# Kernel optimization log

Measured on AMD Instinct MI355X. Metric: run time of the kernel, lower is better.

The kernel has to match this reference:

```python
import jax, jax.numpy as jnp
import numpy as np

B, T, D, H, O = 32, 2048, 256, 512, 256


def setup_inputs() -> dict:
    key = jax.random.key(0)
    ks = jax.random.split(key, 8)
    s = lambda k, shp, fan: jax.random.normal(k, shp, dtype=jnp.float32) / np.sqrt(fan)
    return {
        "x": jax.random.normal(ks[0], (B, T, D), dtype=jnp.float32),
        "h0": jax.random.normal(ks[1], (1, B, H), dtype=jnp.float32),
        "W_ih": s(ks[2], (H, D), D),
        "W_hh": s(ks[3], (H, H), H),
        "b_ih": jnp.zeros((H,), jnp.float32),
        "b_hh": jnp.zeros((H,), jnp.float32),
        "W_lin": s(ks[4], (O, H), H),
        "b_lin": jnp.zeros((O,), jnp.float32),
    }


def reference(x, h0, W_ih, W_hh, b_ih, b_hh, W_lin, b_lin):
    # rnn_act == 'linear' branch: h_t = x_t @ W_ih^T + h_{t-1} @ W_hh^T + b_ih + b_hh
    h_init = h0[0]  # [B, H]
    # Precompute the input contribution for all timesteps at once: [B, T, H]
    xw = jnp.einsum("btd,hd->bth", x, W_ih) + (b_ih + b_hh)

    def step(h, xw_t):  # xw_t: [B, H]
        h_new = xw_t + h @ W_hh.T
        return h_new, h_new

    # scan over time axis
    _, z_t = jax.lax.scan(step, h_init, jnp.swapaxes(xw, 0, 1))  # [T, B, H]
    z = jnp.swapaxes(z_t, 0, 1)  # [B, T, H]

    logits = jnp.einsum("bth,oh->bto", z, W_lin) + b_lin
    out = jax.nn.softmax(logits, axis=2)
    return out, z
```

## Files before the change

kernel.cpp:

```cpp
#include <hip/hip_runtime.h>
#include <math.h>

#define B_ 32
#define T_ 2048
#define D_ 256
#define H_ 512
#define O_ 256
#define S_CH 8
#define C_CH 256

typedef short bf16x8 __attribute__((ext_vector_type(8)));
typedef float f32x4  __attribute__((ext_vector_type(4)));

#define NTL(p)     __builtin_nontemporal_load(p)

__device__ __forceinline__ unsigned short f2bf_rne(float x) {
    unsigned int u = __builtin_bit_cast(unsigned int, x);
    unsigned int r = (u + 0x7fffu + ((u >> 16) & 1u)) >> 16;
    return (unsigned short)r;
}
__device__ __forceinline__ float bf2f(unsigned short h) {
    unsigned int u = ((unsigned int)h) << 16;
    return __builtin_bit_cast(float, u);
}

#define MFMA16(a, b, c) __builtin_amdgcn_mfma_f32_16x16x32_bf16((a), (b), (c), 0, 0, 0)

__device__ __forceinline__ void split_frag(const float* p, bf16x8& hi, bf16x8& lo) {
    f32x4 a = *(const f32x4*)p;
    f32x4 b = *(const f32x4*)(p + 4);
#pragma unroll
    for (int i = 0; i < 4; i++) {
        unsigned short h = f2bf_rne(a[i]);
        hi[i] = (short)h; lo[i] = (short)f2bf_rne(a[i] - bf2f(h));
        unsigned short h2 = f2bf_rne(b[i]);
        hi[4 + i] = (short)h2; lo[4 + i] = (short)f2bf_rne(b[i] - bf2f(h2));
    }
}
__device__ __forceinline__ void split_frag_nt(const float* p, bf16x8& hi, bf16x8& lo) {
    f32x4 a = NTL((const f32x4*)p);
    f32x4 b = NTL((const f32x4*)(p + 4));
#pragma unroll
    for (int i = 0; i < 4; i++) {
        unsigned short h = f2bf_rne(a[i]);
        hi[i] = (short)h; lo[i] = (short)f2bf_rne(a[i] - bf2f(h));
        unsigned short h2 = f2bf_rne(b[i]);
        hi[4 + i] = (short)h2; lo[4 + i] = (short)f2bf_rne(b[i] - bf2f(h2));
    }
}

__device__ __forceinline__ size_t wpack_off(int n, int k, int KB) {
    int n16 = n >> 4, l15 = n & 15;
    int kb = k >> 5, lhi = (k >> 3) & 3, j = k & 7;
    return (((size_t)(n16 * KB + kb) * 4 + lhi) * 16 + l15) * 8 + j;
}

__device__ __forceinline__ int hfrag_off(int m, int n) {
    int m16 = m >> 4, l15m = m & 15;
    int kb = n >> 5, lhi = (n >> 3) & 3, j = n & 7;
    return (((m16 * 16 + kb) * 4 + lhi) * 16 + l15m) * 8 + j;
}

__global__ void k_pack(const float* __restrict__ in, unsigned short* __restrict__ hi,
                       unsigned short* __restrict__ lo, unsigned short* __restrict__ hi2,
                       unsigned short* __restrict__ lo2, int total, int kshift) {
    int i = blockIdx.x * 256 + threadIdx.x;
    if (i < total) {
        int n = i >> kshift;
        int k = i & ((1 << kshift) - 1);
        float v = in[i];
        unsigned short h = f2bf_rne(v);
        unsigned short l = f2bf_rne(v - bf2f(h));
        size_t o = wpack_off(n, k, 1 << (kshift - 5));
        hi[o] = h;
        lo[o] = l;
        if (hi2) { hi2[o] = h; lo2[o] = l; }
    }
}

__device__ __forceinline__ void mul_body(const float* __restrict__ A,
                                         const float* __restrict__ Bm,
                                         float* __restrict__ Out,
                                         unsigned short* __restrict__ d1h,
                                         unsigned short* __restrict__ d1l,
                                         unsigned short* __restrict__ d2h,
                                         unsigned short* __restrict__ d2l,
                                         float (*As)[33], float (*Bs)[33]) {
    int tx = threadIdx.x & 15, ty = threadIdx.x >> 4;
    int j0 = blockIdx.x * 32, i0 = blockIdx.y * 32;
    float a00 = 0.f, a01 = 0.f, a10 = 0.f, a11 = 0.f;
    int r  = threadIdx.x >> 3;
    int c4 = (threadIdx.x & 7) * 4;
    for (int kb = 0; kb < H_ / 32; kb++) {
        f32x4 va = *(const f32x4*)(A + (size_t)(i0 + r) * H_ + kb * 32 + c4);
        f32x4 vb = *(const f32x4*)(Bm + (size_t)(kb * 32 + r) * H_ + j0 + c4);
        __syncthreads();
        As[r][c4 + 0] = va[0]; As[r][c4 + 1] = va[1]; As[r][c4 + 2] = va[2]; As[r][c4 + 3] = va[3];
        Bs[r][c4 + 0] = vb[0]; Bs[r][c4 + 1] = vb[1]; Bs[r][c4 + 2] = vb[2]; Bs[r][c4 + 3] = vb[3];
        __syncthreads();
#pragma unroll
        for (int k = 0; k < 32; k++) {
            float b0 = Bs[k][tx * 2], b1 = Bs[k][tx * 2 + 1];
            float a0 = As[ty * 2][k], a1 = As[ty * 2 + 1][k];
            a00 += a0 * b0; a01 += a0 * b1; a10 += a1 * b0; a11 += a1 * b1;
        }
    }
    float vals[4] = {a00, a01, a10, a11};
#pragma unroll
    for (int q = 0; q < 4; q++) {
        int n = i0 + ty * 2 + (q >> 1);
        int k = j0 + tx * 2 + (q & 1);
        Out[(size_t)n * H_ + k] = vals[q];
        unsigned short h = f2bf_rne(vals[q]);
        unsigned short l = f2bf_rne(vals[q] - bf2f(h));
        size_t o = wpack_off(n, k, 16);
        if (d1h) { d1h[o] = h; d1l[o] = l; }
        if (d2h) { d2h[o] = h; d2l[o] = l; }
    }
}

__global__ __launch_bounds__(256) void k_mul(const float* __restrict__ A,
                                             const float* __restrict__ Bm,
                                             float* __restrict__ Out,
                                             unsigned short* __restrict__ d1h,
                                             unsigned short* __restrict__ d1l,
                                             unsigned short* __restrict__ d2h,
                                             unsigned short* __restrict__ d2l) {
    __shared__ float As[32][33];
    __shared__ float Bs[32][33];
    mul_body(A, Bm, Out, d1h, d1l, d2h, d2l, As, Bs);
}

__global__ __launch_bounds__(256) void k_mul_l2(const float* __restrict__ Whh,
                                                float* __restrict__ ws,
                                                unsigned short* __restrict__ Pp_hi,
                                                unsigned short* __restrict__ Pp_lo) {
    __shared__ float As[32][33];
    __shared__ float Bs[32][33];
    size_t HH = (size_t)H_ * H_;
    if (blockIdx.z == 0)
        mul_body(Whh, ws, ws + HH, Pp_hi + 2 * HH, Pp_lo + 2 * HH, nullptr, nullptr, As, Bs);
    else
        mul_body(ws, ws, ws + 2 * HH, Pp_hi + 3 * HH, Pp_lo + 3 * HH, nullptr, nullptr, As, Bs);
}

__global__ __launch_bounds__(256) void k_mul_l3(const float* __restrict__ Whh,
                                                float* __restrict__ ws,
                                                unsigned short* __restrict__ Pp_hi,
                                                unsigned short* __restrict__ Pp_lo,
                                                unsigned short* __restrict__ Qp_hi,
                                                unsigned short* __restrict__ Qp_lo) {
    __shared__ float As[32][33];
    __shared__ float Bs[32][33];
    size_t HH = (size_t)H_ * H_;
    float* M0 = ws;
    float* M1 = ws + HH;
    float* M2 = ws + 2 * HH;
    int z = blockIdx.z;
    if (z == 0)
        mul_body(Whh, M2, ws + 3 * HH, Pp_hi + 4 * HH, Pp_lo + 4 * HH, nullptr, nullptr, As, Bs);
    else if (z == 1)
        mul_body(M0, M2, ws + 4 * HH, Pp_hi + 5 * HH, Pp_lo + 5 * HH, nullptr, nullptr, As, Bs);
    else if (z == 2)
        mul_body(M1, M2, ws + 5 * HH, Pp_hi + 6 * HH, Pp_lo + 6 * HH, nullptr, nullptr, As, Bs);
    else
        mul_body(M2, M2, ws + 6 * HH, Pp_hi + 7 * HH, Pp_lo + 7 * HH, Qp_hi, Qp_lo, As, Bs);
}

__global__ void k_seed(const float* __restrict__ h0, const float* __restrict__ zb,
                       float* __restrict__ Va) {
    int i = blockIdx.x * 256 + threadIdx.x;
    int c = i >> 14;
    int bn = i & 16383;
    int b = bn >> 9, n = bn & 511;
    Va[i] = (c == 0) ? h0[bn] : zb[((size_t)b * T_ + (c * S_CH - 1)) * H_ + n];
}

__global__ __launch_bounds__(1024) void k_scan2(const float* __restrict__ Vin,
                                                const unsigned short* __restrict__ Qp_hi,
                                                const unsigned short* __restrict__ Qp_lo,
                                                float* __restrict__ Vout, int s) {
    __shared__ __attribute__((aligned(16))) unsigned short hA[16384];
    __shared__ __attribute__((aligned(16))) unsigned short lA[16384];
    int c = blockIdx.x;
    int w = threadIdx.x >> 6;
    int lane = threadIdx.x & 63;
    int l15 = lane & 15, lhi = lane >> 4;

    if (c < s) {
        size_t base = (size_t)c * B_ * H_;
        for (int i = threadIdx.x * 4; i < B_ * H_; i += 4096) {
            f32x4 v = *(const f32x4*)(Vin + base + i);
            *(f32x4*)(Vout + base + i) = v;
        }
        return;
    }

    size_t src = (size_t)(c - s) * B_ * H_;
    for (int i = threadIdx.x; i < 16384; i += 1024) {
        float v = Vin[src + i];
        int m = i >> 9, n = i & 511;
        unsigned short hi = f2bf_rne(v);
        int o = hfrag_off(m, n);
        hA[o] = hi;
        lA[o] = f2bf_rne(v - bf2f(hi));
    }
    __syncthreads();

    size_t dst = (size_t)c * B_ * H_;
    float ad[2][2][4];
#pragma unroll
    for (int mt = 0; mt < 2; mt++)
#pragma unroll
        for (int nt = 0; nt < 2; nt++) {
            int n = w * 32 + nt * 16 + l15;
#pragma unroll
            for (int r = 0; r < 4; r++) {
                int m = mt * 16 + lhi * 4 + r;
                ad[mt][nt][r] = Vin[dst + (size_t)m * H_ + n];
            }
        }

    f32x4 acc[2][2];
#pragma unroll
    for (int mt = 0; mt < 2; mt++)
#pragma unroll
        for (int nt = 0; nt < 2; nt++) acc[mt][nt] = (f32x4){0.f, 0.f, 0.f, 0.f};

    for (int kb = 0; kb < 16; kb++) {
        bf16x8 ah0 = *(const bf16x8*)&hA[(kb << 9) + lane * 8];
        bf16x8 ah1 = *(const bf16x8*)&hA[((16 + kb) << 9) + lane * 8];
        bf16x8 al0 = *(const bf16x8*)&lA[(kb << 9) + lane * 8];
        bf16x8 al1 = *(const bf16x8*)&lA[((16 + kb) << 9) + lane * 8];
#pragma unroll
        for (int nt = 0; nt < 2; nt++) {
            size_t wb = (((size_t)(w * 2 + nt) * 16 + kb) << 9) + lane * 8;
            bf16x8 bh = *(const bf16x8*)(Qp_hi + wb);
            bf16x8 bl = *(const bf16x8*)(Qp_lo + wb);
            acc[0][nt] = MFMA16(ah0, bh, acc[0][nt]);
            acc[0][nt] = MFMA16(al0, bh, acc[0][nt]);
            acc[0][nt] = MFMA16(ah0, bl, acc[0][nt]);
            acc[1][nt] = MFMA16(ah1, bh, acc[1][nt]);
            acc[1][nt] = MFMA16(al1, bh, acc[1][nt]);
            acc[1][nt] = MFMA16(ah1, bl, acc[1][nt]);
        }
    }
#pragma unroll
    for (int mt = 0; mt < 2; mt++)
#pragma unroll
        for (int nt = 0; nt < 2; nt++) {
            int n = w * 32 + nt * 16 + l15;
#pragma unroll
            for (int r = 0; r < 4; r++) {
                int m = mt * 16 + lhi * 4 + r;
                Vout[dst + (size_t)m * H_ + n] = acc[mt][nt][r] + ad[mt][nt][r];
            }
        }
}

__global__ __launch_bounds__(512) void k_xw(const float* __restrict__ x,
                                            const unsigned short* __restrict__ Wp_hi,
                                            const unsigned short* __restrict__ Wp_lo,
                                            const float* __restrict__ bih,
                                            const float* __restrict__ bhh,
                                            float* __restrict__ zb) {
    int b  = blockIdx.y;
    int t0 = blockIdx.x * 64;
    int w    = threadIdx.x >> 6;
    int lane = threadIdx.x & 63;
    int l15 = lane & 15, lhi = lane >> 4;
    int nb = w * 64;

    f32x4 acc[4][4];
    for (int mt = 0; mt < 4; mt++)
        for (int nt = 0; nt < 4; nt++)
            acc[mt][nt] = (f32x4){0.f, 0.f, 0.f, 0.f};

    const float* xb = x + (size_t)b * T_ * D_;
    for (int kb = 0; kb < D_ / 32; kb++) {
        int kofs = kb * 32 + lhi * 8;
        bf16x8 ah[4], al[4];
#pragma unroll
        for (int mt = 0; mt < 4; mt++) {
            int t = t0 + mt * 16 + l15;
            split_frag_nt(xb + (size_t)t * D_ + kofs, ah[mt], al[mt]);
        }
#pragma unroll
        for (int nt = 0; nt < 4; nt++) {
            size_t wb = (((size_t)(w * 4 + nt) * 8 + kb) << 9) + lane * 8;
            bf16x8 bh = *(const bf16x8*)(Wp_hi + wb);
            bf16x8 bl = *(const bf16x8*)(Wp_lo + wb);
#pragma unroll
            for (int mt = 0; mt < 4; mt++) {
                acc[mt][nt] = MFMA16(ah[mt], bh, acc[mt][nt]);
                acc[mt][nt] = MFMA16(al[mt], bh, acc[mt][nt]);
                acc[mt][nt] = MFMA16(ah[mt], bl, acc[mt][nt]);
            }
        }
    }
#pragma unroll
    for (int nt = 0; nt < 4; nt++) {
        int n = nb + nt * 16 + l15;
        float bias = bih[n] + bhh[n];
#pragma unroll
        for (int mt = 0; mt < 4; mt++) {
#pragma unroll
            for (int r = 0; r < 4; r++) {
                int t = t0 + mt * 16 + lhi * 4 + r;
                zb[((size_t)b * T_ + t) * H_ + n] = acc[mt][nt][r] + bias;
            }
        }
    }
}

__global__ __launch_bounds__(1024) void k_phase1(const unsigned short* __restrict__ Wp_hi,
                                                 const unsigned short* __restrict__ Wp_lo,
                                                 float* __restrict__ zb) {
    __shared__ __attribute__((aligned(16))) unsigned short hA[16384];
    __shared__ __attribute__((aligned(16))) unsigned short lA[16384];
    int c = blockIdx.x;
    int w = threadIdx.x >> 6;
    int lane = threadIdx.x & 63;
    int l15 = lane & 15, lhi = lane >> 4;

    bf16x8 wh[2][16], wl[2][16];
#pragma unroll
    for (int nt = 0; nt < 2; nt++)
#pragma unroll
        for (int kb = 0; kb < 16; kb++) {
            size_t wb = (((size_t)(w * 2 + nt) * 16 + kb) << 9) + lane * 8;
            wh[nt][kb] = *(const bf16x8*)(Wp_hi + wb);
            wl[nt][kb] = *(const bf16x8*)(Wp_lo + wb);
        }

    for (int j = 0; j < S_CH; j++) {
        int t = c * S_CH + j;
        float xw[2][2][4];
#pragma unroll
        for (int mt = 0; mt < 2; mt++)
#pragma unroll
            for (int nt = 0; nt < 2; nt++) {
                int n = w * 32 + nt * 16 + l15;
#pragma unroll
                for (int r = 0; r < 4; r++) {
                    int b = mt * 16 + lhi * 4 + r;
                    xw[mt][nt][r] = zb[((size_t)b * T_ + t) * H_ + n];
                }
            }
        f32x4 acc[2][2];
#pragma unroll
        for (int mt = 0; mt < 2; mt++)
#pragma unroll
            for (int nt = 0; nt < 2; nt++) acc[mt][nt] = (f32x4){0.f, 0.f, 0.f, 0.f};
        if (j > 0) {
#pragma unroll
            for (int kb = 0; kb < 16; kb++) {
                bf16x8 ah0 = *(const bf16x8*)&hA[(kb << 9) + lane * 8];
                bf16x8 ah1 = *(const bf16x8*)&hA[((16 + kb) << 9) + lane * 8];
                bf16x8 al0 = *(const bf16x8*)&lA[(kb << 9) + lane * 8];
                bf16x8 al1 = *(const bf16x8*)&lA[((16 + kb) << 9) + lane * 8];
#pragma unroll
                for (int nt = 0; nt < 2; nt++) {
                    acc[0][nt] = MFMA16(ah0, wh[nt][kb], acc[0][nt]);
                    acc[0][nt] = MFMA16(al0, wh[nt][kb], acc[0][nt]);
                    acc[0][nt] = MFMA16(ah0, wl[nt][kb], acc[0][nt]);
                    acc[1][nt] = MFMA16(ah1, wh[nt][kb], acc[1][nt]);
                    acc[1][nt] = MFMA16(al1, wh[nt][kb], acc[1][nt]);
                    acc[1][nt] = MFMA16(ah1, wl[nt][kb], acc[1][nt]);
                }
            }
        }
        __syncthreads();
#pragma unroll
        for (int mt = 0; mt < 2; mt++) {
#pragma unroll
            for (int nt = 0; nt < 2; nt++) {
                int n = w * 32 + nt * 16 + l15;
#pragma unroll
                for (int r = 0; r < 4; r++) {
                    int b = mt * 16 + lhi * 4 + r;
                    float v = acc[mt][nt][r] + xw[mt][nt][r];
                    zb[((size_t)b * T_ + t) * H_ + n] = v;
                    unsigned short hi = f2bf_rne(v);
                    int o = hfrag_off(b, n);
                    hA[o] = hi;
                    lA[o] = f2bf_rne(v - bf2f(hi));
                }
            }
        }
        __syncthreads();
    }
}

__global__ __launch_bounds__(512) void k_carry(const float* __restrict__ Hin,
                                               const unsigned short* __restrict__ Pp_hi,
                                               const unsigned short* __restrict__ Pp_lo,
                                               float* __restrict__ zb) {
    int bid = blockIdx.x;
    int xcd = bid & 7;
    int idx = bid >> 3;
    int mtile  = xcd * 8 + (idx & 7);
    int npanel = idx >> 3;
    int w = threadIdx.x >> 6, lane = threadIdx.x & 63;
    int l15 = lane & 15, lhi = lane >> 4;
    int wm = w >> 2, wn = w & 3;
    int m0 = mtile * 128 + wm * 64;
    int n16base = npanel * 16 + wn * 4;

    f32x4 acc[4][4];
#pragma unroll
    for (int mt = 0; mt < 4; mt++)
#pragma unroll
        for (int nt = 0; nt < 4; nt++) acc[mt][nt] = (f32x4){0.f, 0.f, 0.f, 0.f};

    for (int kb = 0; kb < 16; kb++) {
        int kofs = kb * 32 + lhi * 8;
        bf16x8 ah[4], al[4];
#pragma unroll
        for (int mt = 0; mt < 4; mt++)
            split_frag(Hin + (size_t)(m0 + mt * 16 + l15) * H_ + kofs, ah[mt], al[mt]);
#pragma unroll
        for (int nt = 0; nt < 4; nt++) {
            size_t wb = (((size_t)(n16base + nt) * 16 + kb) << 9) + lane * 8;
            bf16x8 bh = *(const bf16x8*)(Pp_hi + wb);
            bf16x8 bl = *(const bf16x8*)(Pp_lo + wb);
#pragma unroll
            for (int mt = 0; mt < 4; mt++) {
                acc[mt][nt] = MFMA16(ah[mt], bh, acc[mt][nt]);
                acc[mt][nt] = MFMA16(al[mt], bh, acc[mt][nt]);
                acc[mt][nt] = MFMA16(ah[mt], bl, acc[mt][nt]);
            }
        }
    }
#pragma unroll
    for (int nt = 0; nt < 4; nt++) {
        int col = (n16base + nt) * 16 + l15;
        int j = col >> 9, n = col & 511;
#pragma unroll
        for (int mt = 0; mt < 4; mt++) {
#pragma unroll
            for (int r = 0; r < 4; r++) {
                int m = m0 + mt * 16 + lhi * 4 + r;
                int c = m >> 5, b = m & 31;
                size_t zi = ((size_t)b * T_ + (c * S_CH + j)) * H_ + n;
                zb[zi] += acc[mt][nt][r];
            }
        }
    }
}

__global__ __launch_bounds__(256) void k_logits(const float* __restrict__ zq,
                                                const unsigned short* __restrict__ Wp_hi,
                                                const float* __restrict__ blin,
                                                float* __restrict__ out) {
    size_t row0 = (size_t)blockIdx.x * 64;
    int w = threadIdx.x >> 6, lane = threadIdx.x & 63;
    int l15 = lane & 15, lhi = lane >> 4;

    f32x4 acc[16];
#pragma unroll
    for (int nt = 0; nt < 16; nt++) acc[nt] = (f32x4){0.f, 0.f, 0.f, 0.f};

    const float* arow = zq + (row0 + (size_t)w * 16 + l15) * H_;
    for (int kb = 0; kb < 16; kb++) {
        int kofs = kb * 32 + lhi * 8;
        bf16x8 ah, al;
        split_frag_nt(arow + kofs, ah, al);
#pragma unroll
        for (int nt = 0; nt < 16; nt++) {
            size_t wb = (((size_t)nt * 16 + kb) << 9) + lane * 8;
            bf16x8 bh = *(const bf16x8*)(Wp_hi + wb);
            acc[nt] = MFMA16(ah, bh, acc[nt]);
            acc[nt] = MFMA16(al, bh, acc[nt]);
        }
    }
#pragma unroll
    for (int nt = 0; nt < 16; nt++) {
        float bb = blin[nt * 16 + l15];
#pragma unroll
        for (int r = 0; r < 4; r++) acc[nt][r] += bb;
    }
    float rmax[4], rinv[4];
#pragma unroll
    for (int r = 0; r < 4; r++) {
        float mx = -INFINITY;
#pragma unroll
        for (int nt = 0; nt < 16; nt++) mx = fmaxf(mx, acc[nt][r]);
        for (int s = 1; s < 16; s <<= 1) mx = fmaxf(mx, __shfl_xor(mx, s));
        float sum = 0.f;
#pragma unroll
        for (int nt = 0; nt < 16; nt++) sum += __expf(acc[nt][r] - mx);
        for (int s = 1; s < 16; s <<= 1) sum += __shfl_xor(sum, s);
        rmax[r] = mx;
        rinv[r] = 1.f / sum;
    }
#pragma unroll
    for (int nt = 0; nt < 16; nt++) {
#pragma unroll
        for (int r = 0; r < 4; r++) {
            float e = __expf(acc[nt][r] - rmax[r]) * rinv[r];
            size_t row = row0 + (size_t)w * 16 + lhi * 4 + r;
            out[row * O_ + nt * 16 + l15] = e;
        }
    }
}

extern "C" void kernel_launch(void* const* d_in, const int* in_sizes, int n_in,
                              void* d_out, int out_size, void* d_ws, size_t ws_size,
                              hipStream_t stream) {
    const float* x    = (const float*)d_in[0];
    const float* h0   = (const float*)d_in[1];
    const float* Wih  = (const float*)d_in[2];
    const float* Whh  = (const float*)d_in[3];
    const float* bih  = (const float*)d_in[4];
    const float* bhh  = (const float*)d_in[5];
    const float* Wlin = (const float*)d_in[6];
    const float* blin = (const float*)d_in[7];

    float* out  = (float*)d_out;
    float* zout = out + (size_t)B_ * T_ * O_;

    float* ws = (float*)d_ws;
    size_t HH = (size_t)H_ * H_;
    float* M13 = ws + (size_t)13 * HH;
    unsigned short* Wih_hi  = (unsigned short*)(ws + (size_t)14 * HH);
    unsigned short* Wih_lo  = Wih_hi + (size_t)H_ * D_;
    unsigned short* Wlin_hi = Wih_lo + (size_t)H_ * D_;
    unsigned short* Wlin_lo = Wlin_hi + (size_t)O_ * H_;

    float* Va = out;
    float* Vb = out + (size_t)C_CH * B_ * H_;
    unsigned short* Pp_hi = (unsigned short*)((char*)d_out + (size_t)32 * 1024 * 1024);
    unsigned short* Pp_lo = Pp_hi + (size_t)8 * HH;
    unsigned short* Qp_hi = Pp_lo + (size_t)8 * HH;
    unsigned short* Qp_lo = Qp_hi + (size_t)8 * HH;

    unsigned short* nul = nullptr;

    k_pack<<<dim3((H_ * H_) / 256), 256, 0, stream>>>(Whh, Pp_hi, Pp_lo, nul, nul, H_ * H_, 9);
    k_pack<<<dim3((H_ * D_) / 256), 256, 0, stream>>>(Wih, Wih_hi, Wih_lo, nul, nul, H_ * D_, 8);
    k_pack<<<dim3((O_ * H_) / 256), 256, 0, stream>>>(Wlin, Wlin_hi, Wlin_lo, nul, nul, O_ * H_, 9);

    dim3 g16(16, 16);
#define QPH(s) (Qp_hi + (size_t)(s) * HH)
#define QPL(s) (Qp_lo + (size_t)(s) * HH)
    k_mul<<<g16, 256, 0, stream>>>(Whh, Whh, ws, Pp_hi + HH, Pp_lo + HH, nul, nul);
    k_mul_l2<<<dim3(16, 16, 2), 256, 0, stream>>>(Whh, ws, Pp_hi, Pp_lo);
    k_mul_l3<<<dim3(16, 16, 4), 256, 0, stream>>>(Whh, ws, Pp_hi, Pp_lo, Qp_hi, Qp_lo);
    for (int i = 7; i < 14; i++)
        k_mul<<<g16, 256, 0, stream>>>(ws + (size_t)(i - 1) * HH, ws + (size_t)(i - 1) * HH,
                                       ws + (size_t)i * HH, QPH(i - 6), QPL(i - 6), nul, nul);
#undef QPH
#undef QPL
    (void)M13;

    k_xw<<<dim3(T_ / 64, B_), 512, 0, stream>>>(x, Wih_hi, Wih_lo, bih, bhh, zout);

    k_phase1<<<dim3(C_CH), 1024, 0, stream>>>(Pp_hi, Pp_lo, zout);

    k_seed<<<dim3((C_CH * B_ * H_) / 256), 256, 0, stream>>>(h0, zout, Va);
    {
        float* vin = Va;
        float* vout = Vb;
        int s = 1;
        for (int l = 0; l < 8; l++) {
            k_scan2<<<dim3(C_CH), 1024, 0, stream>>>(
                vin, Qp_hi + (size_t)l * HH, Qp_lo + (size_t)l * HH, vout, s);
            float* tmp = vin; vin = vout; vout = tmp;
            s <<= 1;
        }
    }

    k_carry<<<dim3(1024), 512, 0, stream>>>(Va, Pp_hi, Pp_lo, zout);

    k_logits<<<dim3((B_ * T_) / 64), 256, 0, stream>>>(zout, Wlin_hi, blin, out);
}
```

Before: 1.470 ms.

## Emit pre-split bf16 fragments from final scan pass; stream phase1 weights

The last parallel-scan pass now also writes the chunk carry states as pre-split bf16 hi/lo fragments in MFMA layout. k_carry loads these fragments directly instead of re-splitting fp32 rows with split_frag. Separately, k_phase1 stops holding all W fragments in registers and loads them from global memory inside the kb loop, which is no longer unrolled. This lowers register pressure but adds repeated global or cache loads inside the serial time loop. The new scratch buffers sit in the output buffer after Qp.

Result: faster. 1.328 ms (-9.6%).

```diff
diff --git a/kernel.cpp b/kernel.cpp
--- a/kernel.cpp
+++ b/kernel.cpp
@@ -179,19 +179,32 @@
 __global__ __launch_bounds__(1024) void k_scan2(const float* __restrict__ Vin,
                                                 const unsigned short* __restrict__ Qp_hi,
                                                 const unsigned short* __restrict__ Qp_lo,
-                                                float* __restrict__ Vout, int s) {
+                                                float* __restrict__ Vout, int s,
+                                                unsigned short* __restrict__ Ap_hi,
+                                                unsigned short* __restrict__ Ap_lo) {
     __shared__ __attribute__((aligned(16))) unsigned short hA[16384];
     __shared__ __attribute__((aligned(16))) unsigned short lA[16384];
     int c = blockIdx.x;
     int w = threadIdx.x >> 6;
     int lane = threadIdx.x & 63;
     int l15 = lane & 15, lhi = lane >> 4;
+    size_t abase = (size_t)c << 14;
 
     if (c < s) {
         size_t base = (size_t)c * B_ * H_;
         for (int i = threadIdx.x * 4; i < B_ * H_; i += 4096) {
             f32x4 v = *(const f32x4*)(Vin + base + i);
             *(f32x4*)(Vout + base + i) = v;
+            if (Ap_hi) {
+                int m = i >> 9, n = i & 511;
+#pragma unroll
+                for (int q = 0; q < 4; q++) {
+                    unsigned short h = f2bf_rne(v[q]);
+                    size_t o = abase + hfrag_off(m, n + q);
+                    Ap_hi[o] = h;
+                    Ap_lo[o] = f2bf_rne(v[q] - bf2f(h));
+                }
+            }
         }
         return;
     }
@@ -253,7 +266,14 @@
 #pragma unroll
             for (int r = 0; r < 4; r++) {
                 int m = mt * 16 + lhi * 4 + r;
-                Vout[dst + (size_t)m * H_ + n] = acc[mt][nt][r] + ad[mt][nt][r];
+                float v = acc[mt][nt][r] + ad[mt][nt][r];
+                Vout[dst + (size_t)m * H_ + n] = v;
+                if (Ap_hi) {
+                    unsigned short h = f2bf_rne(v);
+                    size_t o = abase + hfrag_off(m, n);
+                    Ap_hi[o] = h;
+                    Ap_lo[o] = f2bf_rne(v - bf2f(h));
+                }
             }
         }
 }
@@ -323,16 +343,6 @@
     int lane = threadIdx.x & 63;
     int l15 = lane & 15, lhi = lane >> 4;
 
-    bf16x8 wh[2][16], wl[2][16];
-#pragma unroll
-    for (int nt = 0; nt < 2; nt++)
-#pragma unroll
-        for (int kb = 0; kb < 16; kb++) {
-            size_t wb = (((size_t)(w * 2 + nt) * 16 + kb) << 9) + lane * 8;
-            wh[nt][kb] = *(const bf16x8*)(Wp_hi + wb);
-            wl[nt][kb] = *(const bf16x8*)(Wp_lo + wb);
-        }
-
     for (int j = 0; j < S_CH; j++) {
         int t = c * S_CH + j;
         float xw[2][2][4];
@@ -353,7 +363,6 @@
 #pragma unroll
             for (int nt = 0; nt < 2; nt++) acc[mt][nt] = (f32x4){0.f, 0.f, 0.f, 0.f};
         if (j > 0) {
-#pragma unroll
             for (int kb = 0; kb < 16; kb++) {
                 bf16x8 ah0 = *(const bf16x8*)&hA[(kb << 9) + lane * 8];
                 bf16x8 ah1 = *(const bf16x8*)&hA[((16 + kb) << 9) + lane * 8];
@@ -361,12 +370,15 @@
                 bf16x8 al1 = *(const bf16x8*)&lA[((16 + kb) << 9) + lane * 8];
 #pragma unroll
                 for (int nt = 0; nt < 2; nt++) {
-                    acc[0][nt] = MFMA16(ah0, wh[nt][kb], acc[0][nt]);
-                    acc[0][nt] = MFMA16(al0, wh[nt][kb], acc[0][nt]);
-                    acc[0][nt] = MFMA16(ah0, wl[nt][kb], acc[0][nt]);
-                    acc[1][nt] = MFMA16(ah1, wh[nt][kb], acc[1][nt]);
-                    acc[1][nt] = MFMA16(al1, wh[nt][kb], acc[1][nt]);
-                    acc[1][nt] = MFMA16(ah1, wl[nt][kb], acc[1][nt]);
+                    size_t wb = (((size_t)(w * 2 + nt) * 16 + kb) << 9) + lane * 8;
+                    bf16x8 bh = *(const bf16x8*)(Wp_hi + wb);
+                    bf16x8 bl = *(const bf16x8*)(Wp_lo + wb);
+                    acc[0][nt] = MFMA16(ah0, bh, acc[0][nt]);
+                    acc[0][nt] = MFMA16(al0, bh, acc[0][nt]);
+                    acc[0][nt] = MFMA16(ah0, bl, acc[0][nt]);
+                    acc[1][nt] = MFMA16(ah1, bh, acc[1][nt]);
+                    acc[1][nt] = MFMA16(al1, bh, acc[1][nt]);
+                    acc[1][nt] = MFMA16(ah1, bl, acc[1][nt]);
                 }
             }
         }
@@ -392,7 +404,8 @@
     }
 }
 
-__global__ __launch_bounds__(512) void k_carry(const float* __restrict__ Hin,
+__global__ __launch_bounds__(512) void k_carry(const unsigned short* __restrict__ Ap_hi,
+                                               const unsigned short* __restrict__ Ap_lo,
                                                const unsigned short* __restrict__ Pp_hi,
                                                const unsigned short* __restrict__ Pp_lo,
                                                float* __restrict__ zb) {
@@ -405,6 +418,7 @@
     int l15 = lane & 15, lhi = lane >> 4;
     int wm = w >> 2, wn = w & 3;
     int m0 = mtile * 128 + wm * 64;
+    int m16b = m0 >> 4;
     int n16base = npanel * 16 + wn * 4;
 
     f32x4 acc[4][4];
@@ -414,11 +428,13 @@
         for (int nt = 0; nt < 4; nt++) acc[mt][nt] = (f32x4){0.f, 0.f, 0.f, 0.f};
 
     for (int kb = 0; kb < 16; kb++) {
-        int kofs = kb * 32 + lhi * 8;
         bf16x8 ah[4], al[4];
 #pragma unroll
-        for (int mt = 0; mt < 4; mt++)
-            split_frag(Hin + (size_t)(m0 + mt * 16 + l15) * H_ + kofs, ah[mt], al[mt]);
+        for (int mt = 0; mt < 4; mt++) {
+            size_t ao = (((size_t)(m16b + mt) * 16 + kb) << 9) + lane * 8;
+            ah[mt] = *(const bf16x8*)(Ap_hi + ao);
+            al[mt] = *(const bf16x8*)(Ap_lo + ao);
+        }
 #pragma unroll
         for (int nt = 0; nt < 4; nt++) {
             size_t wb = (((size_t)(n16base + nt) * 16 + kb) << 9) + lane * 8;
@@ -522,7 +538,6 @@
 
     float* ws = (float*)d_ws;
     size_t HH = (size_t)H_ * H_;
-    float* M13 = ws + (size_t)13 * HH;
     unsigned short* Wih_hi  = (unsigned short*)(ws + (size_t)14 * HH);
     unsigned short* Wih_lo  = Wih_hi + (size_t)H_ * D_;
     unsigned short* Wlin_hi = Wih_lo + (size_t)H_ * D_;
@@ -534,6 +549,8 @@
     unsigned short* Pp_lo = Pp_hi + (size_t)8 * HH;
     unsigned short* Qp_hi = Pp_lo + (size_t)8 * HH;
     unsigned short* Qp_lo = Qp_hi + (size_t)8 * HH;
+    unsigned short* Ap_hi = Qp_lo + (size_t)8 * HH;
+    unsigned short* Ap_lo = Ap_hi + (size_t)C_CH * B_ * H_;
 
     unsigned short* nul = nullptr;
 
@@ -552,7 +569,6 @@
                                        ws + (size_t)i * HH, QPH(i - 6), QPL(i - 6), nul, nul);
 #undef QPH
 #undef QPL
-    (void)M13;
 
     k_xw<<<dim3(T_ / 64, B_), 512, 0, stream>>>(x, Wih_hi, Wih_lo, bih, bhh, zout);
 
@@ -564,14 +580,16 @@
         float* vout = Vb;
         int s = 1;
         for (int l = 0; l < 8; l++) {
+            unsigned short* ah = (l == 7) ? Ap_hi : nul;
+            unsigned short* al = (l == 7) ? Ap_lo : nul;
             k_scan2<<<dim3(C_CH), 1024, 0, stream>>>(
-                vin, Qp_hi + (size_t)l * HH, Qp_lo + (size_t)l * HH, vout, s);
+                vin, Qp_hi + (size_t)l * HH, Qp_lo + (size_t)l * HH, vout, s, ah, al);
             float* tmp = vin; vin = vout; vout = tmp;
             s <<= 1;
         }
     }
 
-    k_carry<<<dim3(1024), 512, 0, stream>>>(Va, Pp_hi, Pp_lo, zout);
+    k_carry<<<dim3(1024), 512, 0, stream>>>(Ap_hi, Ap_lo, Pp_hi, Pp_lo, zout);
 
     k_logits<<<dim3((B_ * T_) / 64), 256, 0, stream>>>(zout, Wlin_hi, blin, out);
 }
```
